# Kernel tuning notes

Hardware: AMD Instinct MI355X
Metric: run time of the kernel (lower is better)

The kernel has to match this reference:

```python
import jax, jax.numpy as jnp
import numpy as np

FT = 0.2  # clip floor (init arg ft)

def _norm_mat(m):
    # matrix / (count of nonzeros along last dim + 1e-30)
    deg = jnp.sum(m != 0, axis=-1, keepdims=True).astype(m.dtype)
    return m / (deg + 1e-30)

def _l2n(x):
    return x / (jnp.linalg.norm(x, axis=-1, keepdims=True) + 1e-30)

def setup_inputs():
    B, L, D, H, O = 2, 2048, 64, 64, 128
    N = 2 * L
    ks = jax.random.split(jax.random.key(0), 30)
    u = lambda i, s: jax.random.uniform(ks[i], s, jnp.float32)
    g = lambda i, s: jax.random.normal(ks[i], s, jnp.float32) * 0.05
    inp = {}
    inp['word_outputs_0'] = g(0, (B, L, D))
    inp['word_outputs_1'] = g(1, (B, L, D))
    inp['node_hidden'] = g(2, (B, D))
    inp['op_embedding'] = g(3, (B, O, D))
    inp['word_exist_sequence'] = (u(4, (B, N)) < 0.8).astype(jnp.float32)
    inp['word_exist_matrix'] = (u(5, (B, N, N)) < 0.8).astype(jnp.float32)
    inp['word_operator'] = (u(6, (B, N, O)) < 0.02).astype(jnp.float32)
    inp['word_word'] = (u(7, (B, N, N)) < 0.01).astype(jnp.float32)
    inp['depend_0'] = (u(8, (B, L, L)) < 0.05).astype(jnp.float32)
    inp['depend_1'] = (u(9, (B, L, L)) < 0.05).astype(jnp.float32)
    inp['goal_word'] = u(10, (B, N))
    names = [('Wg', (D, H)), ('bg', (H,)), ('Wwk', (D, H)), ('bwk', (H,)),
             ('Wws', (D, H)), ('bws', (H,)), ('Wo', (D, D)), ('bo', (D,)),
             ('Wupd', (3 * H, D)), ('bupd', (D,)), ('Wf', (3 * H + D, D)), ('bf', (D,)),
             ('Wf2', (2 * D, D)), ('bf2', (D,)), ('Wout', (D, D)), ('bout', (D,))]
    for i, (nm, s) in enumerate(names):
        inp[nm] = g(11 + i, s)
    return inp

def _forward(w0, w1, nh, opE, wes, wem, wop, ww, d0, d1, gw,
             Wg, bg, Wwk, bwk, Wws, bws, Wo, bo, Wupd, bupd, Wf, bf, Wf2, bf2, Wout, bout):
    all_w = jnp.concatenate([w0, w1], axis=1)                      # [B,N,D]
    goal_trans = (nh @ Wg + bg)[:, None, :]                        # [B,1,H] (broadcast = expand)
    word_g = _l2n(goal_trans * gw[..., None])                      # [B,N,H]
    word_w_k = _l2n(jnp.matmul(_norm_mat(ww * wem), all_w @ Wwk + bwk))
    ws0 = jnp.matmul(_norm_mat(d0), w0 @ Wws + bws)
    ws1 = jnp.matmul(_norm_mat(d1), w1 @ Wws + bws)
    word_w_s = _l2n(jnp.concatenate([ws0, ws1], axis=1))           # [B,N,H]
    neigh = jnp.concatenate([word_g, word_w_k, word_w_s], axis=-1)  # [B,N,3H]
    forget = jax.nn.sigmoid(jnp.concatenate([all_w, word_g, word_w_k, word_w_s], axis=-1) @ Wf + bf)
    word_updated = jnp.maximum(forget, FT) * all_w + (1.0 - forget) * jax.nn.relu(neigh @ Wupd + bupd)
    adj_op = _norm_mat(jnp.swapaxes(wes[..., None] * wop, 1, 2))   # [B,O,N]
    word_op = jnp.matmul(adj_op, word_updated @ Wo + bo)           # [B,O,D]
    forget2 = jax.nn.sigmoid(jnp.concatenate([opE, word_op], axis=-1) @ Wf2 + bf2)
    op_out = jnp.maximum(forget2, FT) * opE + (1.0 - forget2) * jax.nn.relu(word_op @ Wout + bout)
    # original returns (split(word_updated), op_embedding); concat along node axis here
    return jnp.concatenate([word_updated, op_out], axis=1)         # [B,N+O,D]

def reference(word_outputs_0, word_outputs_1, node_hidden, op_embedding,
              word_exist_sequence, word_exist_matrix, word_operator, word_word,
              depend_0, depend_1, goal_word,
              Wg, bg, Wwk, bwk, Wws, bws, Wo, bo, Wupd, bupd, Wf, bf, Wf2, bf2, Wout, bout):
    return _forward(word_outputs_0, word_outputs_1, node_hidden, op_embedding,
                    word_exist_sequence, word_exist_matrix, word_operator, word_word,
                    depend_0, depend_1, goal_word,
                    Wg, bg, Wwk, bwk, Wws, bws, Wo, bo, Wupd, bupd, Wf, bf, Wf2, bf2, Wout, bout)
```

## Files before the change

### kernel.cpp

```cpp
#include <hip/hip_runtime.h>
#include <cstdint>

typedef unsigned short u16;
typedef unsigned long long u64;

__device__ __forceinline__ u16 f2b(float f){
  union { float f; uint32_t i; } v; v.f = f;
  uint32_t r = v.i + 0x7FFFu + ((v.i >> 16) & 1u);
  return (u16)(r >> 16);
}
__device__ __forceinline__ float b2f(u16 u){
  union { uint32_t i; float f; } v; v.i = ((uint32_t)u) << 16; return v.f;
}
__device__ __forceinline__ float sigmoidf(float x){ return 1.0f / (1.0f + __expf(-x)); }

__device__ __forceinline__ void gl_lds4(const void* g, void* l){
  __builtin_amdgcn_global_load_lds((const __attribute__((address_space(1))) void*)g,
                                   (__attribute__((address_space(3))) void*)l, 4, 0, 0);
}
#define WAIT_VM0() __builtin_amdgcn_s_waitcnt(0x0F70)

__global__ __launch_bounds__(256) void k_bits_all(
    const float* __restrict__ ww, const float* __restrict__ wem,
    const float* __restrict__ d0, const float* __restrict__ d1,
    const float* __restrict__ wes, const float* __restrict__ wop,
    const float* __restrict__ w0, const float* __restrict__ w1,
    const float* __restrict__ nh, const float* __restrict__ Wg, const float* __restrict__ bg,
    const float* __restrict__ Wf, const float* __restrict__ Wupd, const float* __restrict__ Wo,
    u16* __restrict__ psumB, int* __restrict__ pcntB,
    u16* __restrict__ psumD, int* __restrict__ pcntD,
    u64* __restrict__ bitOp, float* __restrict__ ghat,
    uint32_t* __restrict__ pkWf, uint32_t* __restrict__ pkWu, uint32_t* __restrict__ pkWo){
  __shared__ int q[4][256];
  __shared__ float rows[4][16][64];
  int tid = threadIdx.x;
  if (blockIdx.x >= 12544){
    int aux = blockIdx.x - 12544;
    if (aux == 16){
      if (tid < 128){
        int b = tid >> 6, h = tid & 63;
        float g = bg[h];
        for (int d = 0; d < 64; ++d) g += nh[b*64 + d] * Wg[d*64 + h];
        float ss = g * g;
        #pragma unroll
        for (int o = 32; o > 0; o >>= 1) ss += __shfl_xor(ss, o, 64);
        ghat[b*64 + h] = g / (sqrtf(ss) + 1e-30f);
      }
      return;
    }
    for (int k = tid; k < 1024; k += 256){
      int i = aux*1024 + k;
      const float* src; uint32_t* dst; int li;
      if (i < 8192){ src = Wf; dst = pkWf; li = i; }
      else if (i < 14336){ src = Wupd; dst = pkWu; li = i - 8192; }
      else { src = Wo; dst = pkWo; li = i - 14336; }
      int k2 = li >> 6, ln = li & 63;
      dst[li] = (uint32_t)f2b(src[(2*k2)*64 + ln]) | ((uint32_t)f2b(src[(2*k2+1)*64 + ln]) << 16);
    }
    return;
  }
  int wave = tid >> 6, lane = tid & 63;
  int wid = blockIdx.x*4 + wave;
  if (wid >= 49152){
    int ng0 = (wid - 49152) * 8;
    #pragma unroll
    for (int i = 0; i < 8; ++i){
      int n = ng0 + i;
      float vx = wop[(size_t)n*128 + lane];
      float vy = wop[(size_t)n*128 + 64 + lane];
      float e  = wes[n];
      u64 m0 = __ballot((e != 0.f) && (vx != 0.f));
      u64 m1 = __ballot((e != 0.f) && (vy != 0.f));
      if (lane == 0) bitOp[(size_t)n*2]     = m0;
      if (lane == 1) bitOp[(size_t)n*2 + 1] = m1;
    }
    return;
  }
  const float *A, *B;
  const float *srcA, *srcB;
  int jbase, thresh;
  u16* ps; int* pc;
  if (wid < 32768){
    int row = wid >> 2, chunk = wid & 3;
    int b = row >> 12;
    A = ww  + (size_t)row*4096 + chunk*1024;
    B = wem + (size_t)row*4096 + chunk*1024;
    srcA = w0 + (size_t)b*131072 + lane;
    srcB = w1 + (size_t)b*131072 - 131072 + lane;
    jbase = chunk*1024; thresh = 2048;
    ps = psumB + (size_t)wid*64; pc = pcntB + wid;
  } else {
    int idx = wid - 32768;
    int rowp = idx >> 1, chunk = idx & 1;
    if (rowp < 4096){
      int b = rowp >> 11;
      A = d0 + (size_t)rowp*2048 + chunk*1024;
      srcA = w0 + (size_t)b*131072 + lane;
    } else {
      int rr = rowp - 4096, b = rr >> 11;
      A = d1 + (size_t)rr*2048 + chunk*1024;
      srcA = w1 + (size_t)b*131072 + lane;
    }
    B = A; srcB = srcA;
    jbase = chunk*1024; thresh = 4096;
    ps = psumD + (size_t)idx*64; pc = pcntD + idx;
  }
  const float4* ap = (const float4*)A + lane;
  const float4* bp = (const float4*)B + lane;
  float4 a0 = ap[0], a1 = ap[64], a2 = ap[128], a3 = ap[192];
  float4 b0 = bp[0], b1 = bp[64], b2 = bp[128], b3 = bp[192];
  u64 myw = 0;
#define B4(i, va, vb) { \
  u64 m0 = __ballot((va.x != 0.f) && (vb.x != 0.f)); \
  u64 m1 = __ballot((va.y != 0.f) && (vb.y != 0.f)); \
  u64 m2 = __ballot((va.z != 0.f) && (vb.z != 0.f)); \
  u64 m3 = __ballot((va.w != 0.f) && (vb.w != 0.f)); \
  if (lane == (i)*4 + 0) myw = m0; \
  if (lane == (i)*4 + 1) myw = m1; \
  if (lane == (i)*4 + 2) myw = m2; \
  if (lane == (i)*4 + 3) myw = m3; }
  B4(0, a0, b0) B4(1, a1, b1) B4(2, a2, b2) B4(3, a3, b3)
#undef B4
  int c = __popcll(myw);
  int pre = c;
  #pragma unroll
  for (int off = 1; off < 64; off <<= 1){
    int t = __shfl_up(pre, off, 64);
    if (lane >= off) pre += t;
  }
  int total = __shfl(pre, 63, 64);
  int base = pre - c;
  int colhi = (lane >> 2) * 256 + (lane & 3);
  u64 m = myw;
  while (m){
    int p = __builtin_ctzll(m); m &= m - 1;
    q[wave][base++] = colhi + p*4;
  }
#define GPJ(qv) (((jbase + (qv)) < thresh ? srcA : srcB) + (size_t)(jbase + (qv))*64)
  float acc = 0.f;
  int i = 0;
  for (; i + 16 <= total; i += 16){
    int4 c0 = *(const int4*)&q[wave][i];
    int4 c1 = *(const int4*)&q[wave][i + 4];
    int4 c2 = *(const int4*)&q[wave][i + 8];
    int4 c3 = *(const int4*)&q[wave][i + 12];
    gl_lds4(GPJ(c0.x), &rows[wave][ 0][0]);
    gl_lds4(GPJ(c0.y), &rows[wave][ 1][0]);
    gl_lds4(GPJ(c0.z), &rows[wave][ 2][0]);
    gl_lds4(GPJ(c0.w), &rows[wave][ 3][0]);
    gl_lds4(GPJ(c1.x), &rows[wave][ 4][0]);
    gl_lds4(GPJ(c1.y), &rows[wave][ 5][0]);
    gl_lds4(GPJ(c1.z), &rows[wave][ 6][0]);
    gl_lds4(GPJ(c1.w), &rows[wave][ 7][0]);
    gl_lds4(GPJ(c2.x), &rows[wave][ 8][0]);
    gl_lds4(GPJ(c2.y), &rows[wave][ 9][0]);
    gl_lds4(GPJ(c2.z), &rows[wave][10][0]);
    gl_lds4(GPJ(c2.w), &rows[wave][11][0]);
    gl_lds4(GPJ(c3.x), &rows[wave][12][0]);
    gl_lds4(GPJ(c3.y), &rows[wave][13][0]);
    gl_lds4(GPJ(c3.z), &rows[wave][14][0]);
    gl_lds4(GPJ(c3.w), &rows[wave][15][0]);
    WAIT_VM0();
    float s0 = 0.f, s1 = 0.f, s2 = 0.f, s3 = 0.f;
    #pragma unroll
    for (int r = 0; r < 4; ++r){
      s0 += rows[wave][r][lane];
      s1 += rows[wave][4 + r][lane];
      s2 += rows[wave][8 + r][lane];
      s3 += rows[wave][12 + r][lane];
    }
    acc += (s0 + s1) + (s2 + s3);
  }
  for (; i < total; ++i) acc += *GPJ(q[wave][i]);
#undef GPJ
  ps[lane] = f2b(acc);
  if (lane == 0) pc[0] = total;
}

__global__ __launch_bounds__(256) void k_fin(
    const u16* __restrict__ psumB, const int* __restrict__ pcntB,
    const u16* __restrict__ psumD, const int* __restrict__ pcntD,
    const float* __restrict__ Wwk, const float* __restrict__ bwk,
    const float* __restrict__ Wws, const float* __restrict__ bws,
    u16* __restrict__ wwkn, u16* __restrict__ wwsn){
  __shared__ float sWk[4096], sWs[4096];
  int tid = threadIdx.x, lane = tid & 63, wave = tid >> 6;
  for (int i = tid; i < 1024; i += 256){
    ((float4*)sWk)[i] = ((const float4*)Wwk)[i];
    ((float4*)sWs)[i] = ((const float4*)Wws)[i];
  }
  __syncthreads();
  int wid = blockIdx.x*4 + wave;
  float S; float y; const float* sW; u16* outp; size_t oidx;
  if (wid < 8192){
    S = b2f(psumB[((size_t)wid*4 + 0)*64 + lane]) + b2f(psumB[((size_t)wid*4 + 1)*64 + lane])
      + b2f(psumB[((size_t)wid*4 + 2)*64 + lane]) + b2f(psumB[((size_t)wid*4 + 3)*64 + lane]);
    int T = pcntB[wid*4] + pcntB[wid*4 + 1] + pcntB[wid*4 + 2] + pcntB[wid*4 + 3];
    y = (float)T * bwk[lane]; sW = sWk; outp = wwkn; oidx = wid;
  } else {
    int rp = wid - 8192;
    S = b2f(psumD[((size_t)rp*2 + 0)*64 + lane]) + b2f(psumD[((size_t)rp*2 + 1)*64 + lane]);
    int T = pcntD[rp*2] + pcntD[rp*2 + 1];
    y = (float)T * bws[lane]; sW = sWs; outp = wwsn;
    int b, n;
    if (rp < 4096){ b = rp >> 11; n = rp & 2047; }
    else { int rr = rp - 4096; b = rr >> 11; n = 2048 + (rr & 2047); }
    oidx = (size_t)b*4096 + n;
  }
  #pragma unroll 8
  for (int d = 0; d < 64; ++d) y += __shfl(S, d, 64) * sW[d*64 + lane];
  float ss = y * y;
  #pragma unroll
  for (int o = 32; o > 0; o >>= 1) ss += __shfl_xor(ss, o, 64);
  outp[oidx*64 + lane] = f2b(y / (sqrtf(ss) + 1e-30f));
}

__global__ __launch_bounds__(256, 2) void k_update(
    const float* __restrict__ w0, const float* __restrict__ w1,
    const float* __restrict__ gw, const float* __restrict__ ghat,
    const u16* __restrict__ wwkn, const u16* __restrict__ wwsn,
    const uint32_t* __restrict__ pkWf, const uint32_t* __restrict__ pkWu,
    const uint32_t* __restrict__ pkWo,
    const float* __restrict__ bf, const float* __restrict__ bupd, const float* __restrict__ bo,
    float* __restrict__ out, float* __restrict__ WUo){
  __shared__ uint32_t pWf[8192];
  __shared__ uint32_t pWu[6144];
  __shared__ uint32_t pWo[2048];
  __shared__ float xsh[4][256];
  int tid = threadIdx.x;
  for (int i = tid; i < 2048; i += 256) ((uint4*)pWf)[i] = ((const uint4*)pkWf)[i];
  for (int i = tid; i < 1536; i += 256) ((uint4*)pWu)[i] = ((const uint4*)pkWu)[i];
  for (int i = tid; i < 512;  i += 256) ((uint4*)pWo)[i] = ((const uint4*)pkWo)[i];
  __syncthreads();
  int lane = tid & 63, wave = tid >> 6;
  float bff = bf[lane], bup = bupd[lane], boo = bo[lane];
  float aw[4], wgv[4], wk[4], wsv[4];
  #pragma unroll
  for (int t = 0; t < 4; ++t){
    int row = blockIdx.x*4 + wave + t*2048;
    int b = row >> 12, n = row & 4095;
    aw[t] = (n < 2048) ? w0[((size_t)(b*2048 + n))*64 + lane]
                       : w1[((size_t)(b*2048 + n - 2048))*64 + lane];
    float gvv = gw[b*4096 + n];
    wgv[t] = (gvv != 0.f) ? ghat[b*64 + lane] : 0.f;
    wk[t]  = b2f(wwkn[(size_t)row*64 + lane]);
    wsv[t] = b2f(wwsn[(size_t)row*64 + lane]);
  }
  #pragma unroll
  for (int t = 0; t < 4; ++t){
    int row = blockIdx.x*4 + wave + t*2048;
    int b = row >> 12, n = row & 4095;
    xsh[wave][lane] = aw[t]; xsh[wave][64 + lane] = wgv[t];
    xsh[wave][128 + lane] = wk[t]; xsh[wave][192 + lane] = wsv[t];
    float f = bff, u = bup;
    #pragma unroll 8
    for (int k2 = 0; k2 < 32; ++k2){
      float2 xv = *(const float2*)&xsh[wave][2*k2];
      uint32_t wf = pWf[k2*64 + lane];
      f += xv.x * b2f((u16)wf) + xv.y * b2f((u16)(wf >> 16));
    }
    #pragma unroll 8
    for (int k2 = 32; k2 < 128; ++k2){
      float2 xv = *(const float2*)&xsh[wave][2*k2];
      uint32_t wf = pWf[k2*64 + lane];
      uint32_t wu = pWu[(k2 - 32)*64 + lane];
      f += xv.x * b2f((u16)wf) + xv.y * b2f((u16)(wf >> 16));
      u += xv.x * b2f((u16)wu) + xv.y * b2f((u16)(wu >> 16));
    }
    f = sigmoidf(f);
    u = fmaxf(u, 0.f);
    float wu = fmaxf(f, 0.2f) * aw[t] + (1.f - f) * u;
    out[((size_t)b*4224 + n)*64 + lane] = wu;
    float o = boo;
    #pragma unroll 8
    for (int k2 = 0; k2 < 32; ++k2){
      uint32_t wo2 = pWo[k2*64 + lane];
      o += __shfl(wu, 2*k2, 64) * b2f((u16)wo2) + __shfl(wu, 2*k2 + 1, 64) * b2f((u16)(wo2 >> 16));
    }
    WUo[(size_t)row*64 + lane] = o;
  }
}

__global__ __launch_bounds__(256) void k_opfin(
    const u64* __restrict__ bitOp, const float* __restrict__ WUo,
    const float* __restrict__ opE,
    const float* __restrict__ Wf2, const float* __restrict__ bf2,
    const float* __restrict__ Wout, const float* __restrict__ bout,
    float* __restrict__ out){
  __shared__ float sW2[8192];
  __shared__ float sWo[4096];
  __shared__ int q[4][96];
  __shared__ float sacc[4][64];
  __shared__ int scnt[4];
  __shared__ float xsh[128];
  int tid = threadIdx.x, lane = tid & 63, wave = tid >> 6;
  for (int i = tid; i < 2048; i += 256) ((float4*)sW2)[i] = ((const float4*)Wf2)[i];
  for (int i = tid; i < 1024; i += 256) ((float4*)sWo)[i] = ((const float4*)Wout)[i];
  int rowIdx = blockIdx.x;
  int b = rowIdx >> 7, o = rowIdx & 127;
  int wrd = o >> 6, bit = o & 63;
  const u64* bp = bitOp + (size_t)b*8192 + (size_t)wave*2048 + wrd;
  u64 lt = (1ULL << lane) - 1ULL;
  u64 vv[16];
  #pragma unroll
  for (int it = 0; it < 16; ++it) vv[it] = bp[(size_t)(it*64 + lane)*2];
  int cnt = 0;
  #pragma unroll
  for (int it = 0; it < 16; ++it){
    bool nz = (vv[it] >> bit) & 1ULL;
    u64 m = __ballot(nz);
    if (nz) q[wave][cnt + (int)__popcll(m & lt)] = wave*1024 + it*64 + lane;
    cnt += (int)__popcll(m);
  }
  const float* Xb = WUo + (size_t)b*4096*64 + lane;
  float acc = 0.f;
  int i = 0;
  for (; i + 8 <= cnt; i += 8){
    int4 c0 = *(const int4*)&q[wave][i];
    int4 c1 = *(const int4*)&q[wave][i + 4];
    float v0 = Xb[(size_t)c0.x*64], v1 = Xb[(size_t)c0.y*64];
    float v2 = Xb[(size_t)c0.z*64], v3 = Xb[(size_t)c0.w*64];
    float v4 = Xb[(size_t)c1.x*64], v5 = Xb[(size_t)c1.y*64];
    float v6 = Xb[(size_t)c1.z*64], v7 = Xb[(size_t)c1.w*64];
    acc += ((v0 + v1) + (v2 + v3)) + ((v4 + v5) + (v6 + v7));
  }
  for (; i < cnt; ++i) acc += Xb[(size_t)q[wave][i]*64];
  sacc[wave][lane] = acc;
  if (lane == 0) scnt[wave] = cnt;
  __syncthreads();
  if (wave == 0){
    float t = sacc[0][lane] + sacc[1][lane] + sacc[2][lane] + sacc[3][lane];
    float deg = (float)(scnt[0] + scnt[1] + scnt[2] + scnt[3]);
    float wo = t / (deg + 1e-30f);
    float e  = opE[(size_t)rowIdx*64 + lane];
    xsh[lane] = e; xsh[64 + lane] = wo;
    float f = bf2[lane], u = bout[lane];
    #pragma unroll 8
    for (int k = 0; k < 128; ++k) f += xsh[k] * sW2[k*64 + lane];
    #pragma unroll 8
    for (int d = 0; d < 64; ++d)  u += xsh[64 + d] * sWo[d*64 + lane];
    f = sigmoidf(f);
    u = fmaxf(u, 0.f);
    float res = fmaxf(f, 0.2f) * e + (1.f - f) * u;
    out[((size_t)b*4224 + 4096 + o)*64 + lane] = res;
  }
}

extern "C" void kernel_launch(void* const* d_in, const int* in_sizes, int n_in,
                              void* d_out, int out_size, void* d_ws, size_t ws_size,
                              hipStream_t stream){
  const float* w0   = (const float*)d_in[0];
  const float* w1   = (const float*)d_in[1];
  const float* nh   = (const float*)d_in[2];
  const float* opE  = (const float*)d_in[3];
  const float* wes  = (const float*)d_in[4];
  const float* wem  = (const float*)d_in[5];
  const float* wop  = (const float*)d_in[6];
  const float* ww   = (const float*)d_in[7];
  const float* d0   = (const float*)d_in[8];
  const float* d1   = (const float*)d_in[9];
  const float* gw   = (const float*)d_in[10];
  const float* Wg   = (const float*)d_in[11];
  const float* bg   = (const float*)d_in[12];
  const float* Wwk  = (const float*)d_in[13];
  const float* bwk  = (const float*)d_in[14];
  const float* Wws  = (const float*)d_in[15];
  const float* bws  = (const float*)d_in[16];
  const float* Wo   = (const float*)d_in[17];
  const float* bo   = (const float*)d_in[18];
  const float* Wupd = (const float*)d_in[19];
  const float* bupd = (const float*)d_in[20];
  const float* Wf   = (const float*)d_in[21];
  const float* bf   = (const float*)d_in[22];
  const float* Wf2  = (const float*)d_in[23];
  const float* bf2  = (const float*)d_in[24];
  const float* Wout = (const float*)d_in[25];
  const float* bout = (const float*)d_in[26];

  float* ws    = (float*)d_ws;
  float* ghat  = ws;
  uint32_t* pkWf = (uint32_t*)(ws + 128);
  uint32_t* pkWu = (uint32_t*)(ws + 8320);
  uint32_t* pkWo = (uint32_t*)(ws + 14464);
  u64*  bitOp  = (u64*)(ws + 16512);
  u16*  psumB  = (u16*)(ws + 49280);
  int*  pcntB  = (int*)(ws + 1097856);
  u16*  psumD  = (u16*)(ws + 1130624);
  int*  pcntD  = (int*)(ws + 1654912);
  u16*  wwkn   = (u16*)(ws + 1671296);
  u16*  wwsn   = (u16*)(ws + 1933440);
  float* WUo   = ws + 2195584;
  float* out   = (float*)d_out;

  k_bits_all<<<12561, 256, 0, stream>>>(ww, wem, d0, d1, wes, wop, w0, w1,
                                        nh, Wg, bg, Wf, Wupd, Wo,
                                        psumB, pcntB, psumD, pcntD,
                                        bitOp, ghat, pkWf, pkWu, pkWo);
  k_fin<<<4096, 256, 0, stream>>>(psumB, pcntB, psumD, pcntD,
                                  Wwk, bwk, Wws, bws, wwkn, wwsn);
  k_update<<<512, 256, 0, stream>>>(w0, w1, gw, ghat, wwkn, wwsn,
                                    pkWf, pkWu, pkWo, bf, bupd, bo, out, WUo);
  k_opfin<<<256, 256, 0, stream>>>(bitOp, WUo, opE, Wf2, bf2, Wout, bout, out);
}
```

Before: 443.4 us.

## Split bitmask streaming from sparse row gather and double-buffer gather loads

The fused kernel is split in two. One kernel streams the dense mask matrices and writes nonzero bitmasks to workspace. A second kernel reads the bitmasks and gathers neighbor rows using a two-stage double-buffered LDS pipeline of 8-row batches with partial vmcnt waits, instead of 16-row batches that fully drain before summing. The depend path also no longer loads the same data twice. The aim is to keep the dense streaming at full bandwidth and overlap gather latency. The cost is an extra launch and an intermediate bitmask round-trip. The bits buffer aliases the wwkn region, which is only written later.

```diff
diff --git a/kernel.cpp b/kernel.cpp
--- a/kernel.cpp
+++ b/kernel.cpp
@@ -18,21 +18,15 @@
   __builtin_amdgcn_global_load_lds((const __attribute__((address_space(1))) void*)g,
                                    (__attribute__((address_space(3))) void*)l, 4, 0, 0);
 }
-#define WAIT_VM0() __builtin_amdgcn_s_waitcnt(0x0F70)
-
-__global__ __launch_bounds__(256) void k_bits_all(
+
+__global__ __launch_bounds__(256) void k_stream(
     const float* __restrict__ ww, const float* __restrict__ wem,
     const float* __restrict__ d0, const float* __restrict__ d1,
     const float* __restrict__ wes, const float* __restrict__ wop,
-    const float* __restrict__ w0, const float* __restrict__ w1,
     const float* __restrict__ nh, const float* __restrict__ Wg, const float* __restrict__ bg,
     const float* __restrict__ Wf, const float* __restrict__ Wupd, const float* __restrict__ Wo,
-    u16* __restrict__ psumB, int* __restrict__ pcntB,
-    u16* __restrict__ psumD, int* __restrict__ pcntD,
-    u64* __restrict__ bitOp, float* __restrict__ ghat,
+    u64* __restrict__ bits, u64* __restrict__ bitOp, float* __restrict__ ghat,
     uint32_t* __restrict__ pkWf, uint32_t* __restrict__ pkWu, uint32_t* __restrict__ pkWo){
-  __shared__ int q[4][256];
-  __shared__ float rows[4][16][64];
   int tid = threadIdx.x;
   if (blockIdx.x >= 12544){
     int aux = blockIdx.x - 12544;
@@ -77,38 +71,25 @@
     return;
   }
   const float *A, *B;
-  const float *srcA, *srcB;
-  int jbase, thresh;
-  u16* ps; int* pc;
+  bool two;
   if (wid < 32768){
     int row = wid >> 2, chunk = wid & 3;
-    int b = row >> 12;
     A = ww  + (size_t)row*4096 + chunk*1024;
     B = wem + (size_t)row*4096 + chunk*1024;
-    srcA = w0 + (size_t)b*131072 + lane;
-    srcB = w1 + (size_t)b*131072 - 131072 + lane;
-    jbase = chunk*1024; thresh = 2048;
-    ps = psumB + (size_t)wid*64; pc = pcntB + wid;
+    two = true;
   } else {
     int idx = wid - 32768;
     int rowp = idx >> 1, chunk = idx & 1;
-    if (rowp < 4096){
-      int b = rowp >> 11;
-      A = d0 + (size_t)rowp*2048 + chunk*1024;
-      srcA = w0 + (size_t)b*131072 + lane;
-    } else {
-      int rr = rowp - 4096, b = rr >> 11;
-      A = d1 + (size_t)rr*2048 + chunk*1024;
-      srcA = w1 + (size_t)b*131072 + lane;
-    }
-    B = A; srcB = srcA;
-    jbase = chunk*1024; thresh = 4096;
-    ps = psumD + (size_t)idx*64; pc = pcntD + idx;
+    if (rowp < 4096) A = d0 + (size_t)rowp*2048 + chunk*1024;
+    else { int rr = rowp - 4096; A = d1 + (size_t)rr*2048 + chunk*1024; }
+    B = A; two = false;
   }
   const float4* ap = (const float4*)A + lane;
   const float4* bp = (const float4*)B + lane;
   float4 a0 = ap[0], a1 = ap[64], a2 = ap[128], a3 = ap[192];
-  float4 b0 = bp[0], b1 = bp[64], b2 = bp[128], b3 = bp[192];
+  float4 b0, b1, b2, b3;
+  if (two){ b0 = bp[0]; b1 = bp[64]; b2 = bp[128]; b3 = bp[192]; }
+  else    { b0 = a0;    b1 = a1;     b2 = a2;      b3 = a3; }
   u64 myw = 0;
 #define B4(i, va, vb) { \
   u64 m0 = __ballot((va.x != 0.f) && (vb.x != 0.f)); \
@@ -121,6 +102,43 @@
   if (lane == (i)*4 + 3) myw = m3; }
   B4(0, a0, b0) B4(1, a1, b1) B4(2, a2, b2) B4(3, a3, b3)
 #undef B4
+  if (lane < 16) bits[(size_t)wid*16 + lane] = myw;
+}
+
+__global__ __launch_bounds__(256) void k_gather(
+    const u64* __restrict__ bits,
+    const float* __restrict__ w0, const float* __restrict__ w1,
+    u16* __restrict__ psumB, int* __restrict__ pcntB,
+    u16* __restrict__ psumD, int* __restrict__ pcntD){
+  __shared__ int q[4][272];
+  __shared__ float rows[4][2][8][64];
+  int tid = threadIdx.x, wave = tid >> 6, lane = tid & 63;
+  int wid = blockIdx.x*4 + wave;
+  const float *srcA, *srcB;
+  int jbase, thresh;
+  u16* ps; int* pc;
+  if (wid < 32768){
+    int row = wid >> 2, chunk = wid & 3;
+    int b = row >> 12;
+    srcA = w0 + (size_t)b*131072 + lane;
+    srcB = w1 + (size_t)b*131072 - 131072 + lane;
+    jbase = chunk*1024; thresh = 2048;
+    ps = psumB + (size_t)wid*64; pc = pcntB + wid;
+  } else {
+    int idx = wid - 32768;
+    int rowp = idx >> 1, chunk = idx & 1;
+    if (rowp < 4096){
+      int b = rowp >> 11;
+      srcA = w0 + (size_t)b*131072 + lane;
+    } else {
+      int rr = rowp - 4096, b = rr >> 11;
+      srcA = w1 + (size_t)b*131072 + lane;
+    }
+    srcB = srcA;
+    jbase = chunk*1024; thresh = 4096;
+    ps = psumD + (size_t)idx*64; pc = pcntD + idx;
+  }
+  u64 myw = (lane < 16) ? bits[(size_t)wid*16 + lane] : 0ULL;
   int c = __popcll(myw);
   int pre = c;
   #pragma unroll
@@ -136,42 +154,41 @@
     int p = __builtin_ctzll(m); m &= m - 1;
     q[wave][base++] = colhi + p*4;
   }
+  int totP = (total + 7) & ~7;
+  if (lane < totP - total) q[wave][total + lane] = 0;
+  float acc = 0.f;
+  int nb = totP >> 3;
 #define GPJ(qv) (((jbase + (qv)) < thresh ? srcA : srcB) + (size_t)(jbase + (qv))*64)
-  float acc = 0.f;
-  int i = 0;
-  for (; i + 16 <= total; i += 16){
-    int4 c0 = *(const int4*)&q[wave][i];
-    int4 c1 = *(const int4*)&q[wave][i + 4];
-    int4 c2 = *(const int4*)&q[wave][i + 8];
-    int4 c3 = *(const int4*)&q[wave][i + 12];
-    gl_lds4(GPJ(c0.x), &rows[wave][ 0][0]);
-    gl_lds4(GPJ(c0.y), &rows[wave][ 1][0]);
-    gl_lds4(GPJ(c0.z), &rows[wave][ 2][0]);
-    gl_lds4(GPJ(c0.w), &rows[wave][ 3][0]);
-    gl_lds4(GPJ(c1.x), &rows[wave][ 4][0]);
-    gl_lds4(GPJ(c1.y), &rows[wave][ 5][0]);
-    gl_lds4(GPJ(c1.z), &rows[wave][ 6][0]);
-    gl_lds4(GPJ(c1.w), &rows[wave][ 7][0]);
-    gl_lds4(GPJ(c2.x), &rows[wave][ 8][0]);
-    gl_lds4(GPJ(c2.y), &rows[wave][ 9][0]);
-    gl_lds4(GPJ(c2.z), &rows[wave][10][0]);
-    gl_lds4(GPJ(c2.w), &rows[wave][11][0]);
-    gl_lds4(GPJ(c3.x), &rows[wave][12][0]);
-    gl_lds4(GPJ(c3.y), &rows[wave][13][0]);
-    gl_lds4(GPJ(c3.z), &rows[wave][14][0]);
-    gl_lds4(GPJ(c3.w), &rows[wave][15][0]);
-    WAIT_VM0();
-    float s0 = 0.f, s1 = 0.f, s2 = 0.f, s3 = 0.f;
-    #pragma unroll
-    for (int r = 0; r < 4; ++r){
-      s0 += rows[wave][r][lane];
-      s1 += rows[wave][4 + r][lane];
-      s2 += rows[wave][8 + r][lane];
-      s3 += rows[wave][12 + r][lane];
-    }
-    acc += (s0 + s1) + (s2 + s3);
-  }
-  for (; i < total; ++i) acc += *GPJ(q[wave][i]);
+#define ISSUE(bi, bsel) { \
+  int4 c0 = *(const int4*)&q[wave][(bi)*8]; \
+  int4 c1 = *(const int4*)&q[wave][(bi)*8 + 4]; \
+  gl_lds4(GPJ(c0.x), &rows[wave][bsel][0][0]); \
+  gl_lds4(GPJ(c0.y), &rows[wave][bsel][1][0]); \
+  gl_lds4(GPJ(c0.z), &rows[wave][bsel][2][0]); \
+  gl_lds4(GPJ(c0.w), &rows[wave][bsel][3][0]); \
+  gl_lds4(GPJ(c1.x), &rows[wave][bsel][4][0]); \
+  gl_lds4(GPJ(c1.y), &rows[wave][bsel][5][0]); \
+  gl_lds4(GPJ(c1.z), &rows[wave][bsel][6][0]); \
+  gl_lds4(GPJ(c1.w), &rows[wave][bsel][7][0]); }
+  if (nb > 0){
+    ISSUE(0, 0)
+    if (nb > 1) ISSUE(1, 1)
+    for (int b = 0; b < nb; ++b){
+      if (b + 1 < nb){ asm volatile("s_waitcnt vmcnt(8)" ::: "memory"); }
+      else           { asm volatile("s_waitcnt vmcnt(0)" ::: "memory"); }
+      int bs = b & 1;
+      #pragma unroll
+      for (int r = 0; r < 8; ++r){
+        float v = rows[wave][bs][r][lane];
+        acc += (b*8 + r < total) ? v : 0.f;
+      }
+      if (b + 2 < nb){
+        asm volatile("s_waitcnt lgkmcnt(0)" ::: "memory");
+        ISSUE(b + 2, bs)
+      }
+    }
+  }
+#undef ISSUE
 #undef GPJ
   ps[lane] = f2b(acc);
   if (lane == 0) pc[0] = total;
@@ -390,12 +407,14 @@
   u16*  wwkn   = (u16*)(ws + 1671296);
   u16*  wwsn   = (u16*)(ws + 1933440);
   float* WUo   = ws + 2195584;
+  u64*  bits   = (u64*)(ws + 1671296);
   float* out   = (float*)d_out;
 
-  k_bits_all<<<12561, 256, 0, stream>>>(ww, wem, d0, d1, wes, wop, w0, w1,
-                                        nh, Wg, bg, Wf, Wupd, Wo,
-                                        psumB, pcntB, psumD, pcntD,
-                                        bitOp, ghat, pkWf, pkWu, pkWo);
+  k_stream<<<12561, 256, 0, stream>>>(ww, wem, d0, d1, wes, wop,
+                                      nh, Wg, bg, Wf, Wupd, Wo,
+                                      bits, bitOp, ghat, pkWf, pkWu, pkWo);
+  k_gather<<<12288, 256, 0, stream>>>(bits, w0, w1,
+                                      psumB, pcntB, psumD, pcntD);
   k_fin<<<4096, 256, 0, stream>>>(psumB, pcntB, psumD, pcntD,
                                   Wwk, bwk, Wws, bws, wwkn, wwsn);
   k_update<<<512, 256, 0, stream>>>(w0, w1, gw, ghat, wwkn, wwsn,
```

Measured after the change: 468.5 us. 1.06x slower.

## Make mask kernel persistent with prefetch of next tile's mask rows

Applied to the files above, without the earlier changes.

The mask/gather kernel now has each wave process six work items in a loop. The next item's mask rows are loaded while the current item's gather-sum runs, instead of one item per wave across a huge grid. The gather loop now handles batches of 8 padded indices with masked accumulation rather than 16 plus a scalar tail. k_fin likewise has each wave handle four rows, so the grid shrinks. This is meant to hide mask-load latency and cut launch and scheduling overhead, at the cost of fewer resident waves and extra registers for the prefetch.

```diff
diff --git a/kernel.cpp b/kernel.cpp
--- a/kernel.cpp
+++ b/kernel.cpp
@@ -18,9 +18,25 @@
   __builtin_amdgcn_global_load_lds((const __attribute__((address_space(1))) void*)g,
                                    (__attribute__((address_space(3))) void*)l, 4, 0, 0);
 }
-#define WAIT_VM0() __builtin_amdgcn_s_waitcnt(0x0F70)
-
-__global__ __launch_bounds__(256) void k_bits_all(
+
+__device__ __forceinline__ void mask_ptrs(int t,
+    const float* ww, const float* wem, const float* d0, const float* d1,
+    const float4** ap, const float4** bp, bool* two){
+  if (t < 32768){
+    int row = t >> 2, chunk = t & 3;
+    *ap = (const float4*)(ww  + (size_t)row*4096 + chunk*1024);
+    *bp = (const float4*)(wem + (size_t)row*4096 + chunk*1024);
+    *two = true;
+  } else {
+    int idx = t - 32768, rowp = idx >> 1, chunk = idx & 1;
+    const float* base;
+    if (rowp < 4096) base = d0 + (size_t)rowp*2048 + chunk*1024;
+    else { int rr = rowp - 4096; base = d1 + (size_t)rr*2048 + chunk*1024; }
+    *ap = (const float4*)base; *bp = (const float4*)base; *two = false;
+  }
+}
+
+__global__ __launch_bounds__(256) void k_mask(
     const float* __restrict__ ww, const float* __restrict__ wem,
     const float* __restrict__ d0, const float* __restrict__ d1,
     const float* __restrict__ wes, const float* __restrict__ wop,
@@ -31,38 +47,38 @@
     u16* __restrict__ psumD, int* __restrict__ pcntD,
     u64* __restrict__ bitOp, float* __restrict__ ghat,
     uint32_t* __restrict__ pkWf, uint32_t* __restrict__ pkWu, uint32_t* __restrict__ pkWo){
-  __shared__ int q[4][256];
-  __shared__ float rows[4][16][64];
-  int tid = threadIdx.x;
-  if (blockIdx.x >= 12544){
-    int aux = blockIdx.x - 12544;
-    if (aux == 16){
-      if (tid < 128){
-        int b = tid >> 6, h = tid & 63;
-        float g = bg[h];
-        for (int d = 0; d < 64; ++d) g += nh[b*64 + d] * Wg[d*64 + h];
-        float ss = g * g;
-        #pragma unroll
-        for (int o = 32; o > 0; o >>= 1) ss += __shfl_xor(ss, o, 64);
-        ghat[b*64 + h] = g / (sqrtf(ss) + 1e-30f);
+  __shared__ int q[4][272];
+  __shared__ float rows[4][8][64];
+  int tid = threadIdx.x, wave = tid >> 6, lane = tid & 63;
+  int bid = blockIdx.x;
+  if (bid >= 2048){
+    if (bid >= 2304){
+      int aux = bid - 2304;
+      if (aux == 16){
+        if (tid < 128){
+          int b = tid >> 6, h = tid & 63;
+          float g = bg[h];
+          for (int d = 0; d < 64; ++d) g += nh[b*64 + d] * Wg[d*64 + h];
+          float ss = g * g;
+          #pragma unroll
+          for (int o = 32; o > 0; o >>= 1) ss += __shfl_xor(ss, o, 64);
+          ghat[b*64 + h] = g / (sqrtf(ss) + 1e-30f);
+        }
+        return;
+      }
+      for (int k = tid; k < 1024; k += 256){
+        int i = aux*1024 + k;
+        const float* src; uint32_t* dst; int li;
+        if (i < 8192){ src = Wf; dst = pkWf; li = i; }
+        else if (i < 14336){ src = Wupd; dst = pkWu; li = i - 8192; }
+        else { src = Wo; dst = pkWo; li = i - 14336; }
+        int k2 = li >> 6, ln = li & 63;
+        dst[li] = (uint32_t)f2b(src[(2*k2)*64 + ln]) | ((uint32_t)f2b(src[(2*k2+1)*64 + ln]) << 16);
       }
       return;
     }
-    for (int k = tid; k < 1024; k += 256){
-      int i = aux*1024 + k;
-      const float* src; uint32_t* dst; int li;
-      if (i < 8192){ src = Wf; dst = pkWf; li = i; }
-      else if (i < 14336){ src = Wupd; dst = pkWu; li = i - 8192; }
-      else { src = Wo; dst = pkWo; li = i - 14336; }
-      int k2 = li >> 6, ln = li & 63;
-      dst[li] = (uint32_t)f2b(src[(2*k2)*64 + ln]) | ((uint32_t)f2b(src[(2*k2+1)*64 + ln]) << 16);
-    }
-    return;
-  }
-  int wave = tid >> 6, lane = tid & 63;
-  int wid = blockIdx.x*4 + wave;
-  if (wid >= 49152){
-    int ng0 = (wid - 49152) * 8;
+    int w = (bid - 2048)*4 + wave;
+    int ng0 = w * 8;
     #pragma unroll
     for (int i = 0; i < 8; ++i){
       int n = ng0 + i;
@@ -76,105 +92,105 @@
     }
     return;
   }
-  const float *A, *B;
-  const float *srcA, *srcB;
-  int jbase, thresh;
-  u16* ps; int* pc;
-  if (wid < 32768){
-    int row = wid >> 2, chunk = wid & 3;
-    int b = row >> 12;
-    A = ww  + (size_t)row*4096 + chunk*1024;
-    B = wem + (size_t)row*4096 + chunk*1024;
-    srcA = w0 + (size_t)b*131072 + lane;
-    srcB = w1 + (size_t)b*131072 - 131072 + lane;
-    jbase = chunk*1024; thresh = 2048;
-    ps = psumB + (size_t)wid*64; pc = pcntB + wid;
-  } else {
-    int idx = wid - 32768;
-    int rowp = idx >> 1, chunk = idx & 1;
-    if (rowp < 4096){
-      int b = rowp >> 11;
-      A = d0 + (size_t)rowp*2048 + chunk*1024;
+  int wid = bid*4 + wave;
+  const float4 *ap, *bp; bool two;
+  mask_ptrs(wid, ww, wem, d0, d1, &ap, &bp, &two);
+  float4 a0 = ap[lane], a1 = ap[64 + lane], a2 = ap[128 + lane], a3 = ap[192 + lane];
+  float4 b0 = {0,0,0,0}, b1 = {0,0,0,0}, b2 = {0,0,0,0}, b3 = {0,0,0,0};
+  if (two){ b0 = bp[lane]; b1 = bp[64 + lane]; b2 = bp[128 + lane]; b3 = bp[192 + lane]; }
+
+  for (int it = 0; it < 6; ++it){
+    int t = wid + it*8192;
+    const float *srcA, *srcB;
+    int jbase, thresh;
+    u16* ps; int* pc;
+    if (t < 32768){
+      int row = t >> 2, chunk = t & 3;
+      int b = row >> 12;
       srcA = w0 + (size_t)b*131072 + lane;
+      srcB = w1 + (size_t)b*131072 - 131072 + lane;
+      jbase = chunk*1024; thresh = 2048;
+      ps = psumB + (size_t)t*64; pc = pcntB + t;
     } else {
-      int rr = rowp - 4096, b = rr >> 11;
-      A = d1 + (size_t)rr*2048 + chunk*1024;
-      srcA = w1 + (size_t)b*131072 + lane;
-    }
-    B = A; srcB = srcA;
-    jbase = chunk*1024; thresh = 4096;
-    ps = psumD + (size_t)idx*64; pc = pcntD + idx;
-  }
-  const float4* ap = (const float4*)A + lane;
-  const float4* bp = (const float4*)B + lane;
-  float4 a0 = ap[0], a1 = ap[64], a2 = ap[128], a3 = ap[192];
-  float4 b0 = bp[0], b1 = bp[64], b2 = bp[128], b3 = bp[192];
-  u64 myw = 0;
+      int idx = t - 32768, rowp = idx >> 1, chunk = idx & 1;
+      if (rowp < 4096){
+        int b = rowp >> 11;
+        srcA = w0 + (size_t)b*131072 + lane;
+      } else {
+        int rr = rowp - 4096, b = rr >> 11;
+        srcA = w1 + (size_t)b*131072 + lane;
+      }
+      srcB = srcA;
+      jbase = chunk*1024; thresh = 4096;
+      ps = psumD + (size_t)idx*64; pc = pcntD + idx;
+    }
+    float4 an0 = {0,0,0,0}, an1 = {0,0,0,0}, an2 = {0,0,0,0}, an3 = {0,0,0,0};
+    float4 bn0 = {0,0,0,0}, bn1 = {0,0,0,0}, bn2 = {0,0,0,0}, bn3 = {0,0,0,0};
+    bool twon = false;
+    if (it < 5){
+      const float4 *apn, *bpn;
+      mask_ptrs(t + 8192, ww, wem, d0, d1, &apn, &bpn, &twon);
+      an0 = apn[lane]; an1 = apn[64 + lane]; an2 = apn[128 + lane]; an3 = apn[192 + lane];
+      if (twon){ bn0 = bpn[lane]; bn1 = bpn[64 + lane]; bn2 = bpn[128 + lane]; bn3 = bpn[192 + lane]; }
+    }
+    u64 myw = 0;
 #define B4(i, va, vb) { \
-  u64 m0 = __ballot((va.x != 0.f) && (vb.x != 0.f)); \
-  u64 m1 = __ballot((va.y != 0.f) && (vb.y != 0.f)); \
-  u64 m2 = __ballot((va.z != 0.f) && (vb.z != 0.f)); \
-  u64 m3 = __ballot((va.w != 0.f) && (vb.w != 0.f)); \
+  u64 m0 = __ballot((va.x != 0.f) && (!two || (vb.x != 0.f))); \
+  u64 m1 = __ballot((va.y != 0.f) && (!two || (vb.y != 0.f))); \
+  u64 m2 = __ballot((va.z != 0.f) && (!two || (vb.z != 0.f))); \
+  u64 m3 = __ballot((va.w != 0.f) && (!two || (vb.w != 0.f))); \
   if (lane == (i)*4 + 0) myw = m0; \
   if (lane == (i)*4 + 1) myw = m1; \
   if (lane == (i)*4 + 2) myw = m2; \
   if (lane == (i)*4 + 3) myw = m3; }
-  B4(0, a0, b0) B4(1, a1, b1) B4(2, a2, b2) B4(3, a3, b3)
+    B4(0, a0, b0) B4(1, a1, b1) B4(2, a2, b2) B4(3, a3, b3)
 #undef B4
-  int c = __popcll(myw);
-  int pre = c;
-  #pragma unroll
-  for (int off = 1; off < 64; off <<= 1){
-    int t = __shfl_up(pre, off, 64);
-    if (lane >= off) pre += t;
-  }
-  int total = __shfl(pre, 63, 64);
-  int base = pre - c;
-  int colhi = (lane >> 2) * 256 + (lane & 3);
-  u64 m = myw;
-  while (m){
-    int p = __builtin_ctzll(m); m &= m - 1;
-    q[wave][base++] = colhi + p*4;
-  }
+    int c = __popcll(myw);
+    int pre = c;
+    #pragma unroll
+    for (int off = 1; off < 64; off <<= 1){
+      int tt = __shfl_up(pre, off, 64);
+      if (lane >= off) pre += tt;
+    }
+    int total = __shfl(pre, 63, 64);
+    int base = pre - c;
+    int colhi = (lane >> 2) * 256 + (lane & 3);
+    u64 m = myw;
+    while (m){
+      int p = __builtin_ctzll(m); m &= m - 1;
+      q[wave][base++] = colhi + p*4;
+    }
+    int totP = (total + 7) & ~7;
+    if (lane < totP - total) q[wave][total + lane] = 0;
+    float acc = 0.f;
 #define GPJ(qv) (((jbase + (qv)) < thresh ? srcA : srcB) + (size_t)(jbase + (qv))*64)
-  float acc = 0.f;
-  int i = 0;
-  for (; i + 16 <= total; i += 16){
-    int4 c0 = *(const int4*)&q[wave][i];
-    int4 c1 = *(const int4*)&q[wave][i + 4];
-    int4 c2 = *(const int4*)&q[wave][i + 8];
-    int4 c3 = *(const int4*)&q[wave][i + 12];
-    gl_lds4(GPJ(c0.x), &rows[wave][ 0][0]);
-    gl_lds4(GPJ(c0.y), &rows[wave][ 1][0]);
-    gl_lds4(GPJ(c0.z), &rows[wave][ 2][0]);
-    gl_lds4(GPJ(c0.w), &rows[wave][ 3][0]);
-    gl_lds4(GPJ(c1.x), &rows[wave][ 4][0]);
-    gl_lds4(GPJ(c1.y), &rows[wave][ 5][0]);
-    gl_lds4(GPJ(c1.z), &rows[wave][ 6][0]);
-    gl_lds4(GPJ(c1.w), &rows[wave][ 7][0]);
-    gl_lds4(GPJ(c2.x), &rows[wave][ 8][0]);
-    gl_lds4(GPJ(c2.y), &rows[wave][ 9][0]);
-    gl_lds4(GPJ(c2.z), &rows[wave][10][0]);
-    gl_lds4(GPJ(c2.w), &rows[wave][11][0]);
-    gl_lds4(GPJ(c3.x), &rows[wave][12][0]);
-    gl_lds4(GPJ(c3.y), &rows[wave][13][0]);
-    gl_lds4(GPJ(c3.z), &rows[wave][14][0]);
-    gl_lds4(GPJ(c3.w), &rows[wave][15][0]);
-    WAIT_VM0();
-    float s0 = 0.f, s1 = 0.f, s2 = 0.f, s3 = 0.f;
-    #pragma unroll
-    for (int r = 0; r < 4; ++r){
-      s0 += rows[wave][r][lane];
-      s1 += rows[wave][4 + r][lane];
-      s2 += rows[wave][8 + r][lane];
-      s3 += rows[wave][12 + r][lane];
-    }
-    acc += (s0 + s1) + (s2 + s3);
-  }
-  for (; i < total; ++i) acc += *GPJ(q[wave][i]);
+    for (int b8 = 0; b8 < totP; b8 += 8){
+      int4 c0 = *(const int4*)&q[wave][b8];
+      int4 c1 = *(const int4*)&q[wave][b8 + 4];
+      gl_lds4(GPJ(c0.x), &rows[wave][0][0]);
+      gl_lds4(GPJ(c0.y), &rows[wave][1][0]);
+      gl_lds4(GPJ(c0.z), &rows[wave][2][0]);
+      gl_lds4(GPJ(c0.w), &rows[wave][3][0]);
+      gl_lds4(GPJ(c1.x), &rows[wave][4][0]);
+      gl_lds4(GPJ(c1.y), &rows[wave][5][0]);
+      gl_lds4(GPJ(c1.z), &rows[wave][6][0]);
+      gl_lds4(GPJ(c1.w), &rows[wave][7][0]);
+      asm volatile("s_waitcnt vmcnt(0)" ::: "memory");
+      #pragma unroll
+      for (int r = 0; r < 8; ++r){
+        float v = rows[wave][r][lane];
+        acc += (b8 + r < total) ? v : 0.f;
+      }
+    }
 #undef GPJ
-  ps[lane] = f2b(acc);
-  if (lane == 0) pc[0] = total;
+    ps[lane] = f2b(acc);
+    if (lane == 0) pc[0] = total;
+    if (it < 5){
+      a0 = an0; a1 = an1; a2 = an2; a3 = an3;
+      if (twon){ b0 = bn0; b1 = bn1; b2 = bn2; b3 = bn3; }
+      two = twon;
+    }
+  }
 }
 
 __global__ __launch_bounds__(256) void k_fin(
@@ -190,29 +206,31 @@
     ((float4*)sWs)[i] = ((const float4*)Wws)[i];
   }
   __syncthreads();
-  int wid = blockIdx.x*4 + wave;
-  float S; float y; const float* sW; u16* outp; size_t oidx;
-  if (wid < 8192){
-    S = b2f(psumB[((size_t)wid*4 + 0)*64 + lane]) + b2f(psumB[((size_t)wid*4 + 1)*64 + lane])
-      + b2f(psumB[((size_t)wid*4 + 2)*64 + lane]) + b2f(psumB[((size_t)wid*4 + 3)*64 + lane]);
-    int T = pcntB[wid*4] + pcntB[wid*4 + 1] + pcntB[wid*4 + 2] + pcntB[wid*4 + 3];
-    y = (float)T * bwk[lane]; sW = sWk; outp = wwkn; oidx = wid;
-  } else {
-    int rp = wid - 8192;
-    S = b2f(psumD[((size_t)rp*2 + 0)*64 + lane]) + b2f(psumD[((size_t)rp*2 + 1)*64 + lane]);
-    int T = pcntD[rp*2] + pcntD[rp*2 + 1];
-    y = (float)T * bws[lane]; sW = sWs; outp = wwsn;
-    int b, n;
-    if (rp < 4096){ b = rp >> 11; n = rp & 2047; }
-    else { int rr = rp - 4096; b = rr >> 11; n = 2048 + (rr & 2047); }
-    oidx = (size_t)b*4096 + n;
-  }
-  #pragma unroll 8
-  for (int d = 0; d < 64; ++d) y += __shfl(S, d, 64) * sW[d*64 + lane];
-  float ss = y * y;
-  #pragma unroll
-  for (int o = 32; o > 0; o >>= 1) ss += __shfl_xor(ss, o, 64);
-  outp[oidx*64 + lane] = f2b(y / (sqrtf(ss) + 1e-30f));
+  for (int r = 0; r < 4; ++r){
+    int wid = blockIdx.x*4 + wave + r*4096;
+    float S; float y; const float* sW; u16* outp; size_t oidx;
+    if (wid < 8192){
+      S = b2f(psumB[((size_t)wid*4 + 0)*64 + lane]) + b2f(psumB[((size_t)wid*4 + 1)*64 + lane])
+        + b2f(psumB[((size_t)wid*4 + 2)*64 + lane]) + b2f(psumB[((size_t)wid*4 + 3)*64 + lane]);
+      int T = pcntB[wid*4] + pcntB[wid*4 + 1] + pcntB[wid*4 + 2] + pcntB[wid*4 + 3];
+      y = (float)T * bwk[lane]; sW = sWk; outp = wwkn; oidx = wid;
+    } else {
+      int rp = wid - 8192;
+      S = b2f(psumD[((size_t)rp*2 + 0)*64 + lane]) + b2f(psumD[((size_t)rp*2 + 1)*64 + lane]);
+      int T = pcntD[rp*2] + pcntD[rp*2 + 1];
+      y = (float)T * bws[lane]; sW = sWs; outp = wwsn;
+      int b, n;
+      if (rp < 4096){ b = rp >> 11; n = rp & 2047; }
+      else { int rr = rp - 4096; b = rr >> 11; n = 2048 + (rr & 2047); }
+      oidx = (size_t)b*4096 + n;
+    }
+    #pragma unroll 8
+    for (int d = 0; d < 64; ++d) y += __shfl(S, d, 64) * sW[d*64 + lane];
+    float ss = y * y;
+    #pragma unroll
+    for (int o = 32; o > 0; o >>= 1) ss += __shfl_xor(ss, o, 64);
+    outp[oidx*64 + lane] = f2b(y / (sqrtf(ss) + 1e-30f));
+  }
 }
 
 __global__ __launch_bounds__(256, 2) void k_update(
@@ -392,11 +410,11 @@
   float* WUo   = ws + 2195584;
   float* out   = (float*)d_out;
 
-  k_bits_all<<<12561, 256, 0, stream>>>(ww, wem, d0, d1, wes, wop, w0, w1,
-                                        nh, Wg, bg, Wf, Wupd, Wo,
-                                        psumB, pcntB, psumD, pcntD,
-                                        bitOp, ghat, pkWf, pkWu, pkWo);
-  k_fin<<<4096, 256, 0, stream>>>(psumB, pcntB, psumD, pcntD,
+  k_mask<<<2321, 256, 0, stream>>>(ww, wem, d0, d1, wes, wop, w0, w1,
+                                   nh, Wg, bg, Wf, Wupd, Wo,
+                                   psumB, pcntB, psumD, pcntD,
+                                   bitOp, ghat, pkWf, pkWu, pkWo);
+  k_fin<<<1024, 256, 0, stream>>>(psumB, pcntB, psumD, pcntD,
                                   Wwk, bwk, Wws, bws, wwkn, wwsn);
   k_update<<<512, 256, 0, stream>>>(w0, w1, gw, ghat, wwkn, wwsn,
                                     pkWf, pkWu, pkWo, bf, bupd, bo, out, WUo);
```

Result: no change. 448.9 us (+1.2%).
